# Performance work log

Measured on AMD Instinct MI355X. Metric: run time of the kernel, lower is better.

Reference implementation:

```python
import jax, jax.numpy as jnp
import numpy as np

LN_EPS = 1e-5
N_HEADS = 8

def _layernorm(x, g, b):
    mu = jnp.mean(x, axis=-1, keepdims=True)
    var = jnp.var(x, axis=-1, keepdims=True)
    return (x - mu) * jax.lax.rsqrt(var + LN_EPS) * g + b

def _posenc(seqlen, d_model, dtype):
    den = jnp.exp(-jnp.arange(0, d_model, 2, dtype=dtype) * (np.log(10000.0) / d_model))
    pos = jnp.arange(seqlen, dtype=dtype)[:, None]  # [S,1]
    pe = jnp.zeros((seqlen, d_model), dtype=dtype)
    pe = pe.at[:, 0::2].set(jnp.sin(pos * den))
    pe = pe.at[:, 1::2].set(jnp.cos(pos * den)[:, : d_model // 2])
    return pe  # [S,d]

def setup_inputs() -> dict:
    key = jax.random.key(0)
    ks = jax.random.split(key, 12)
    B, S, V, D, F, L, DL = 64, 256, 16, 512, 2048, 6, 256
    s = 0.05
    return {
        "src_pad": jax.random.normal(ks[0], (B, S, V), jnp.float32),
        "emb_w": jax.random.normal(ks[1], (D, V), jnp.float32) * s,
        "emb_b": jnp.zeros((D,), jnp.float32),
        "qkv_w": jax.random.normal(ks[2], (L, 3 * D, D), jnp.float32) * s,
        "qkv_b": jnp.zeros((L, 3 * D), jnp.float32),
        "out_w": jax.random.normal(ks[3], (L, D, D), jnp.float32) * s,
        "out_b": jnp.zeros((L, D), jnp.float32),
        "ff1_w": jax.random.normal(ks[4], (L, F, D), jnp.float32) * s,
        "ff1_b": jnp.zeros((L, F), jnp.float32),
        "ff2_w": jax.random.normal(ks[5], (L, D, F), jnp.float32) * s,
        "ff2_b": jnp.zeros((L, D), jnp.float32),
        "ln1_g": jnp.ones((L, D), jnp.float32),
        "ln1_b": jnp.zeros((L, D), jnp.float32),
        "ln2_g": jnp.ones((L, D), jnp.float32),
        "ln2_b": jnp.zeros((L, D), jnp.float32),
        "lat_w": jax.random.normal(ks[6], (DL, S * D), jnp.float32) * 0.005,
        "lat_b": jnp.zeros((DL,), jnp.float32),
        "head_w": jax.random.normal(ks[7], (1, DL), jnp.float32) * s,
        "head_b": jnp.zeros((1,), jnp.float32),
    }

def reference(src_pad, emb_w, emb_b, qkv_w, qkv_b, out_w, out_b,
              ff1_w, ff1_b, ff2_w, ff2_b, ln1_g, ln1_b, ln2_g, ln2_b,
              lat_w, lat_b, head_w, head_b):
    B, S, V = src_pad.shape
    D = emb_w.shape[0]
    L = qkv_w.shape[0]
    H = N_HEADS
    dh = D // H
    # batched replacement of the per-token Python-loop embedding
    x = jnp.einsum('bsv,dv->bsd', src_pad, emb_w) + emb_b
    x = x + _posenc(S, D, x.dtype)  # dropout is identity at eval
    scale = 1.0 / np.sqrt(dh)
    for l in range(L):  # post-norm PyTorch TransformerEncoderLayer, relu FFN
        qkv = jnp.einsum('bsd,ed->bse', x, qkv_w[l]) + qkv_b[l]  # [B,S,3D]
        q, k, v = jnp.split(qkv, 3, axis=-1)
        q = q.reshape(B, S, H, dh).transpose(0, 2, 1, 3)
        k = k.reshape(B, S, H, dh).transpose(0, 2, 1, 3)
        v = v.reshape(B, S, H, dh).transpose(0, 2, 1, 3)
        attn = jax.nn.softmax(jnp.einsum('bhqd,bhkd->bhqk', q, k) * scale, axis=-1)
        o = jnp.einsum('bhqk,bhkd->bhqd', attn, v).transpose(0, 2, 1, 3).reshape(B, S, D)
        o = jnp.einsum('bsd,ed->bse', o, out_w[l]) + out_b[l]
        x = _layernorm(x + o, ln1_g[l], ln1_b[l])
        h = jax.nn.relu(jnp.einsum('bsd,fd->bsf', x, ff1_w[l]) + ff1_b[l])
        h = jnp.einsum('bsf,df->bsd', h, ff2_w[l]) + ff2_b[l]
        x = _layernorm(x + h, ln2_g[l], ln2_b[l])
    mem = x.reshape(B, S * D) @ lat_w.T + lat_b  # [B, d_latent]
    pred = jax.nn.sigmoid(mem @ head_w.T + head_b)  # [B,1]
    return pred
```

## Files before the change

kernel.cpp:

```cpp
#include <hip/hip_runtime.h>
#include <hip/hip_bf16.h>
#include <cstdint>

#define DEV static __device__ __forceinline__

typedef __attribute__((ext_vector_type(8))) short bf16x8;
typedef __attribute__((ext_vector_type(4))) float f32x4;

DEV unsigned short f2bf(float f) {
  union { float f; unsigned u; } c; c.f = f;
  unsigned u = c.u;
  return (unsigned short)((u + 0x7fffu + ((u >> 16) & 1u)) >> 16);
}
DEV float bf2f(unsigned short h) {
  union { unsigned u; float f; } c; c.u = ((unsigned)h) << 16; return c.f;
}
DEV float bflo(unsigned u) { union { unsigned u; float f; } c; c.u = u << 16; return c.f; }
DEV float bfhi(unsigned u) { union { unsigned u; float f; } c; c.u = u & 0xffff0000u; return c.f; }
DEV unsigned pack_bf16(float a, float b) {
  union { float f; unsigned u; } ca, cb; ca.f = a; cb.f = b;
  return __builtin_amdgcn_perm(cb.u + 0x8000u, ca.u + 0x8000u, 0x07060302u);
}

#define ASYNC_COPY16(gsrc, ldst)                                                      \
  __builtin_amdgcn_global_load_lds(                                                   \
      (const __attribute__((address_space(1))) void*)(unsigned long long)(gsrc),      \
      (__attribute__((address_space(3))) void*)(unsigned int)(unsigned long long)(ldst), \
      16, 0, 0)

__global__ void cvt4_kernel(const float* __restrict__ s, unsigned short* __restrict__ d) {
  size_t i = ((size_t)blockIdx.x * 256 + threadIdx.x) * 4;
  float4 v = *(const float4*)(s + i);
  d[i + 0] = f2bf(v.x);
  d[i + 1] = f2bf(v.y);
  d[i + 2] = f2bf(v.z);
  d[i + 3] = f2bf(v.w);
}

__global__ void embed_kernel(const float* __restrict__ src,
                             const float* __restrict__ emb_w,
                             const float* __restrict__ emb_b,
                             unsigned short* __restrict__ xb) {
  const int bs = blockIdx.x;
  const int d = threadIdx.x;
  const int s = bs & 255;
  __shared__ float sv[16];
  if (d < 16) sv[d] = src[(size_t)bs * 16 + d];
  __syncthreads();
  const float* wr = emb_w + (size_t)d * 16;
  float acc = emb_b[d];
#pragma unroll
  for (int v = 0; v < 16; v++) acc += sv[v] * wr[v];
  const float den = __expf(-(float)(d & ~1) * (9.2103403719761836f / 512.f));
  const float arg = (float)s * den;
  acc += (d & 1) ? __cosf(arg) : __sinf(arg);
  xb[(size_t)bs * 512 + d] = f2bf(acc);
}

template <int BM, int RELU, int OUT_BF16, int ADD_RES>
__global__ __launch_bounds__(512, 2) void gemm_pipe(
    const unsigned short* __restrict__ A,
    const unsigned short* __restrict__ B,
    const float* __restrict__ bias,
    const unsigned short* __restrict__ res,
    float* __restrict__ Cf,
    unsigned short* __restrict__ Cb,
    int M, int N, int K) {
  constexpr int BN = 256;
  constexpr int MT = BM / 32;
  constexpr int NT = 4;
  constexpr int NLA = BM / 64;
  constexpr int NL = NLA + BN / 64;
  constexpr int BUFE = (BM + BN) * 64;
  __shared__ unsigned short lds[3 * BUFE];

  const int tid = threadIdx.x;
  const int lane = tid & 63;
  const int w = tid >> 6;
  const int wmi = w >> 2;
  const int wni = w & 3;
  const int r16 = lane & 15;
  const int quad = lane >> 4;
  const int rsw = r16 & 7;
  const int m0 = blockIdx.x * BM;
  const int n0 = blockIdx.y * BN;

  const int srow = tid >> 3;
  const int scol = ((tid & 7) ^ (srow & 7)) * 8;
  const unsigned short* gA = A + (size_t)(m0 + srow) * K + scol;
  const unsigned short* gB = B + (size_t)(n0 + srow) * K + scol;

#define STG(i, bufi, kc)                                                        \
  do {                                                                          \
    if ((i) < NLA)                                                              \
      ASYNC_COPY16(gA + (size_t)((i) * 64) * K + (kc),                          \
                   lds + (bufi) * BUFE + ((i) * 64 + w * 8) * 64);              \
    else                                                                        \
      ASYNC_COPY16(gB + (size_t)(((i) - NLA) * 64) * K + (kc),                  \
                   lds + (bufi) * BUFE + (BM + ((i) - NLA) * 64 + w * 8) * 64); \
  } while (0)

  f32x4 acc[MT][NT] = {};

  const int NK = K >> 6;
#pragma unroll
  for (int i = 0; i < NL; ++i) STG(i, 0, 0);
#pragma unroll
  for (int i = 0; i < NL; ++i) STG(i, 1, 64);

  for (int kt = 0; kt < NK; ++kt) {
    const int buf = kt % 3;
    if (kt + 1 < NK)
      asm volatile("s_waitcnt vmcnt(%0)" ::"i"(NL) : "memory");
    else
      asm volatile("s_waitcnt vmcnt(0)" ::: "memory");
    __builtin_amdgcn_s_barrier();
    if (kt + 2 < NK) {
      const int sb = (kt + 2) % 3;
      const int kc = (kt + 2) << 6;
#pragma unroll
      for (int i = 0; i < NL; ++i) STG(i, sb, kc);
    }
    const unsigned short* As = lds + buf * BUFE;
    const unsigned short* Bs = As + BM * 64;
#pragma unroll
    for (int kh = 0; kh < 2; ++kh) {
      const int ko = ((kh * 4 + quad) ^ rsw) * 8;
      bf16x8 aR[MT], bR[NT];
#pragma unroll
      for (int m = 0; m < MT; ++m)
        aR[m] = *(const bf16x8*)(As + (wmi * 64 + m * 16 + r16) * 64 + ko);
#pragma unroll
      for (int j = 0; j < NT; ++j)
        bR[j] = *(const bf16x8*)(Bs + (wni * 64 + j * 16 + r16) * 64 + ko);
      __builtin_amdgcn_s_setprio(1);
#pragma unroll
      for (int m = 0; m < MT; ++m)
#pragma unroll
        for (int j = 0; j < NT; ++j)
          acc[m][j] = __builtin_amdgcn_mfma_f32_16x16x32_bf16(
              bR[j], aR[m], acc[m][j], 0, 0, 0);
      __builtin_amdgcn_s_setprio(0);
    }
    asm volatile("s_waitcnt lgkmcnt(0)" ::: "memory");
  }
#undef STG

  const int mb = m0 + wmi * 64 + r16;
  const int nb = n0 + wni * 64 + quad * 4;
#pragma unroll
  for (int j = 0; j < NT; ++j) {
    const int n = nb + j * 16;
    const float4 bv = *(const float4*)(bias + n);
#pragma unroll
    for (int i = 0; i < MT; ++i) {
      const size_t off = (size_t)(mb + i * 16) * N + n;
      float4 v;
      v.x = acc[i][j][0] + bv.x;
      v.y = acc[i][j][1] + bv.y;
      v.z = acc[i][j][2] + bv.z;
      v.w = acc[i][j][3] + bv.w;
      if (ADD_RES) {
        const uint2 ru = *(const uint2*)(res + off);
        v.x += bflo(ru.x); v.y += bfhi(ru.x);
        v.z += bflo(ru.y); v.w += bfhi(ru.y);
      }
      if (RELU) {
        v.x = fmaxf(v.x, 0.f); v.y = fmaxf(v.y, 0.f);
        v.z = fmaxf(v.z, 0.f); v.w = fmaxf(v.w, 0.f);
      }
      if (OUT_BF16) {
        uint2 u;
        u.x = pack_bf16(v.x, v.y);
        u.y = pack_bf16(v.z, v.w);
        *(uint2*)(Cb + off) = u;
      } else {
        *(float4*)(Cf + off) = v;
      }
    }
  }
}

__global__ __launch_bounds__(256, 2) void attn_fused(
    const unsigned short* __restrict__ qkv,
    unsigned short* __restrict__ O) {
  __shared__ unsigned short Vt[64 * 264];
  __shared__ unsigned short Pl[32 * 264];
  __shared__ float redM[4][32];
  __shared__ float redS[4][32];
  const int tid = threadIdx.x;
  const int lane = tid & 63;
  const int w = tid >> 6;
  const int r16 = lane & 15;
  const int quad = lane >> 4;
  const int h = blockIdx.x & 7;
  const int b = blockIdx.x >> 3;

  {
    const int kp = w * 32 + (lane & 31);
    const int dhalf = lane >> 5;
    const unsigned short* vbase =
        qkv + (size_t)(b * 256 + 2 * kp) * 1536 + 1024 + h * 64;
    unsigned* dst = (unsigned*)Vt;
#pragma unroll
    for (int t = 0; t < 4; t++) {
      const int dc = dhalf + 2 * t;
      const uint4 a = *(const uint4*)(vbase + dc * 8);
      const uint4 bb = *(const uint4*)(vbase + 1536 + dc * 8);
      const unsigned* ap = (const unsigned*)&a;
      const unsigned* bp = (const unsigned*)&bb;
#pragma unroll
      for (int i = 0; i < 4; i++) {
        const unsigned lo = ap[i], hi = bp[i];
        dst[(dc * 8 + 2 * i) * 132 + kp] = (lo & 0xffffu) | (hi << 16);
        dst[(dc * 8 + 2 * i + 1) * 132 + kp] = (lo >> 16) | (hi & 0xffff0000u);
      }
    }
  }
  __syncthreads();

  const unsigned short* krow =
      qkv + (size_t)(b * 256 + r16) * 1536 + 512 + h * 64 + quad * 8;
  const unsigned short* qrow =
      qkv + (size_t)(b * 256 + r16) * 1536 + h * 64 + quad * 8;

  for (int qt = 0; qt < 8; qt++) {
    const int q0 = qt * 32;
    f32x4 acc[4][2] = {};
    bf16x8 bQ0[2], bQ1[2];
#pragma unroll
    for (int nt = 0; nt < 2; nt++) {
      const unsigned short* qp = qrow + (size_t)(q0 + nt * 16) * 1536;
      bQ0[nt] = *(const bf16x8*)(qp);
      bQ1[nt] = *(const bf16x8*)(qp + 32);
    }
#pragma unroll
    for (int mt = 0; mt < 4; mt++) {
      const unsigned short* kp = krow + (size_t)(w * 64 + mt * 16) * 1536;
      const bf16x8 aK0 = *(const bf16x8*)(kp);
      const bf16x8 aK1 = *(const bf16x8*)(kp + 32);
#pragma unroll
      for (int nt = 0; nt < 2; nt++) {
        acc[mt][nt] = __builtin_amdgcn_mfma_f32_16x16x32_bf16(aK0, bQ0[nt], acc[mt][nt], 0, 0, 0);
        acc[mt][nt] = __builtin_amdgcn_mfma_f32_16x16x32_bf16(aK1, bQ1[nt], acc[mt][nt], 0, 0, 0);
      }
    }
#pragma unroll
    for (int nt = 0; nt < 2; nt++) {
      float m = acc[0][nt][0];
#pragma unroll
      for (int mt = 0; mt < 4; mt++)
#pragma unroll
        for (int r = 0; r < 4; r++) m = fmaxf(m, acc[mt][nt][r]);
      m = fmaxf(m, __shfl_xor(m, 16));
      m = fmaxf(m, __shfl_xor(m, 32));
      if (quad == 0) redM[w][nt * 16 + r16] = m;
    }
    __syncthreads();
    float mg[2], sw[2];
#pragma unroll
    for (int nt = 0; nt < 2; nt++) {
      const int q = nt * 16 + r16;
      mg[nt] = fmaxf(fmaxf(redM[0][q], redM[1][q]), fmaxf(redM[2][q], redM[3][q]));
      sw[nt] = 0.f;
    }
#pragma unroll
    for (int mt = 0; mt < 4; mt++)
#pragma unroll
      for (int nt = 0; nt < 2; nt++)
#pragma unroll
        for (int r = 0; r < 4; r++) {
          acc[mt][nt][r] = __expf((acc[mt][nt][r] - mg[nt]) * 0.125f);
          sw[nt] += acc[mt][nt][r];
        }
#pragma unroll
    for (int nt = 0; nt < 2; nt++) {
      sw[nt] += __shfl_xor(sw[nt], 16);
      sw[nt] += __shfl_xor(sw[nt], 32);
      if (quad == 0) redS[w][nt * 16 + r16] = sw[nt];
    }
    __syncthreads();
    float inv[2];
#pragma unroll
    for (int nt = 0; nt < 2; nt++) {
      const int q = nt * 16 + r16;
      inv[nt] = 1.f / (redS[0][q] + redS[1][q] + redS[2][q] + redS[3][q]);
    }
#pragma unroll
    for (int nt = 0; nt < 2; nt++) {
      unsigned short* prow = Pl + (nt * 16 + r16) * 264 + w * 64 + quad * 4;
#pragma unroll
      for (int mt = 0; mt < 4; mt++) {
        uint2 u;
        u.x = pack_bf16(acc[mt][nt][0] * inv[nt], acc[mt][nt][1] * inv[nt]);
        u.y = pack_bf16(acc[mt][nt][2] * inv[nt], acc[mt][nt][3] * inv[nt]);
        *(uint2*)(prow + mt * 16) = u;
      }
    }
    __syncthreads();
    f32x4 o[2] = {};
#pragma unroll
    for (int s = 0; s < 8; s++) {
      const bf16x8 aV = *(const bf16x8*)(Vt + (w * 16 + r16) * 264 + s * 32 + quad * 8);
#pragma unroll
      for (int nt = 0; nt < 2; nt++) {
        const bf16x8 bP = *(const bf16x8*)(Pl + (nt * 16 + r16) * 264 + s * 32 + quad * 8);
        o[nt] = __builtin_amdgcn_mfma_f32_16x16x32_bf16(aV, bP, o[nt], 0, 0, 0);
      }
    }
#pragma unroll
    for (int nt = 0; nt < 2; nt++) {
      uint2 u;
      u.x = pack_bf16(o[nt][0], o[nt][1]);
      u.y = pack_bf16(o[nt][2], o[nt][3]);
      *(uint2*)(O + (size_t)(b * 256 + q0 + nt * 16 + r16) * 512 + h * 64 +
                w * 16 + quad * 4) = u;
    }
  }
}

__global__ __launch_bounds__(256) void ln_kernel(
    const float* __restrict__ z, const float* __restrict__ g,
    const float* __restrict__ bb, unsigned short* __restrict__ xb) {
  const int row = blockIdx.x;
  const int tid = threadIdx.x;
  const size_t base = (size_t)row * 512;
  float v0 = z[base + tid];
  float v1 = z[base + tid + 256];
  float s = v0 + v1, ss = v0 * v0 + v1 * v1;
#pragma unroll
  for (int off = 32; off > 0; off >>= 1) {
    s += __shfl_xor(s, off);
    ss += __shfl_xor(ss, off);
  }
  __shared__ float red[8];
  const int w = tid >> 6, lane = tid & 63;
  if (lane == 0) { red[w * 2] = s; red[w * 2 + 1] = ss; }
  __syncthreads();
  s = red[0] + red[2] + red[4] + red[6];
  ss = red[1] + red[3] + red[5] + red[7];
  const float mu = s * (1.f / 512.f);
  const float var = ss * (1.f / 512.f) - mu * mu;
  const float rs = rsqrtf(var + 1e-5f);
  const float o0 = (v0 - mu) * rs * g[tid] + bb[tid];
  const float o1 = (v1 - mu) * rs * g[tid + 256] + bb[tid + 256];
  xb[base + tid] = f2bf(o0);
  xb[base + tid + 256] = f2bf(o1);
}

__global__ void zero_kernel(float* __restrict__ p) {
  p[blockIdx.x * 256 + threadIdx.x] = 0.f;
}

__global__ __launch_bounds__(256) void latent_gemm(
    const unsigned short* __restrict__ xb, const float* __restrict__ W,
    float* __restrict__ mem) {
  const int tid = threadIdx.x;
  const int lane = tid & 63;
  const int w = tid >> 6;
  const int r16 = lane & 15;
  const int quad = lane >> 4;
  const int n0 = blockIdx.x * 64 + w * 16;
  const int kc0 = blockIdx.y * 1024;

  const float* wrow = W + (size_t)(n0 + r16) * 131072 + kc0 + quad * 8;
  const unsigned short* xrow = xb + (size_t)r16 * 131072 + kc0 + quad * 8;

  f32x4 c[4] = {};
  for (int k = 0; k < 1024; k += 32) {
    const float4 wa = *(const float4*)(wrow + k);
    const float4 wb = *(const float4*)(wrow + k + 4);
    union { unsigned u[4]; bf16x8 v; } cw;
    cw.u[0] = pack_bf16(wa.x, wa.y);
    cw.u[1] = pack_bf16(wa.z, wa.w);
    cw.u[2] = pack_bf16(wb.x, wb.y);
    cw.u[3] = pack_bf16(wb.z, wb.w);
#pragma unroll
    for (int i = 0; i < 4; i++) {
      const bf16x8 aX = *(const bf16x8*)(xrow + (size_t)i * 2097152 + k);
      c[i] = __builtin_amdgcn_mfma_f32_16x16x32_bf16(aX, cw.v, c[i], 0, 0, 0);
    }
  }
#pragma unroll
  for (int i = 0; i < 4; i++)
#pragma unroll
    for (int r = 0; r < 4; r++)
      atomicAdd(&mem[(size_t)(i * 16 + quad * 4 + r) * 256 + n0 + r16], c[i][r]);
}

__global__ __launch_bounds__(256) void head_kernel(
    const float* __restrict__ mem, const float* __restrict__ lat_b,
    const float* __restrict__ head_w, const float* __restrict__ head_b,
    float* __restrict__ out) {
  const int b = blockIdx.x;
  const int tid = threadIdx.x;
  float v = (mem[(size_t)b * 256 + tid] + lat_b[tid]) * head_w[tid];
#pragma unroll
  for (int off = 32; off > 0; off >>= 1) v += __shfl_xor(v, off);
  __shared__ float red[4];
  const int w = tid >> 6, lane = tid & 63;
  if (lane == 0) red[w] = v;
  __syncthreads();
  if (tid == 0) {
    const float z = red[0] + red[1] + red[2] + red[3] + head_b[0];
    out[b] = 1.f / (1.f + __expf(-z));
  }
}

extern "C" void kernel_launch(void* const* d_in, const int* in_sizes, int n_in,
                              void* d_out, int out_size, void* d_ws, size_t ws_size,
                              hipStream_t stream) {
  (void)in_sizes; (void)n_in; (void)out_size; (void)ws_size;
  const float* src_pad = (const float*)d_in[0];
  const float* emb_w = (const float*)d_in[1];
  const float* emb_b = (const float*)d_in[2];
  const float* qkv_w = (const float*)d_in[3];
  const float* qkv_b = (const float*)d_in[4];
  const float* out_w = (const float*)d_in[5];
  const float* out_b = (const float*)d_in[6];
  const float* ff1_w = (const float*)d_in[7];
  const float* ff1_b = (const float*)d_in[8];
  const float* ff2_w = (const float*)d_in[9];
  const float* ff2_b = (const float*)d_in[10];
  const float* ln1_g = (const float*)d_in[11];
  const float* ln1_b = (const float*)d_in[12];
  const float* ln2_g = (const float*)d_in[13];
  const float* ln2_b = (const float*)d_in[14];
  const float* lat_w = (const float*)d_in[15];
  const float* lat_b = (const float*)d_in[16];
  const float* head_w = (const float*)d_in[17];
  const float* head_b = (const float*)d_in[18];
  float* out = (float*)d_out;

  char* p = (char*)d_ws;
  unsigned short* xb = (unsigned short*)p; p += (size_t)16384 * 512 * 2;
  unsigned short* qkv = (unsigned short*)p;
  float* y = (float*)qkv;
  p += (size_t)16384 * 1536 * 2;
  unsigned short* attno = (unsigned short*)p; p += (size_t)16384 * 512 * 2;
  unsigned short* h = (unsigned short*)p;     p += (size_t)16384 * 2048 * 2;
  unsigned short* wq = (unsigned short*)p;    p += (size_t)4718592 * 2;
  unsigned short* wo = (unsigned short*)p;    p += (size_t)1572864 * 2;
  unsigned short* wf1 = (unsigned short*)p;   p += (size_t)6291456 * 2;
  unsigned short* wf2 = (unsigned short*)p;   p += (size_t)6291456 * 2;
  float* mem = (float*)p;           p += (size_t)16384 * 4;

  cvt4_kernel<<<4608, 256, 0, stream>>>(qkv_w, wq);
  cvt4_kernel<<<1536, 256, 0, stream>>>(out_w, wo);
  cvt4_kernel<<<6144, 256, 0, stream>>>(ff1_w, wf1);
  cvt4_kernel<<<6144, 256, 0, stream>>>(ff2_w, wf2);

  embed_kernel<<<16384, 512, 0, stream>>>(src_pad, emb_w, emb_b, xb);

  for (int l = 0; l < 6; l++) {
    gemm_pipe<128, 0, 1, 0><<<dim3(128, 6), 512, 0, stream>>>(
        xb, wq + (size_t)l * 786432, qkv_b + (size_t)l * 1536, nullptr,
        nullptr, qkv, 16384, 1536, 512);
    attn_fused<<<512, 256, 0, stream>>>(qkv, attno);
    gemm_pipe<128, 0, 0, 1><<<dim3(128, 2), 512, 0, stream>>>(
        attno, wo + (size_t)l * 262144, out_b + (size_t)l * 512, xb,
        y, nullptr, 16384, 512, 512);
    ln_kernel<<<16384, 256, 0, stream>>>(y, ln1_g + (size_t)l * 512,
                                         ln1_b + (size_t)l * 512, xb);
    gemm_pipe<128, 1, 1, 0><<<dim3(128, 8), 512, 0, stream>>>(
        xb, wf1 + (size_t)l * 1048576, ff1_b + (size_t)l * 2048, nullptr,
        nullptr, h, 16384, 2048, 512);
    gemm_pipe<128, 0, 0, 1><<<dim3(128, 2), 512, 0, stream>>>(
        h, wf2 + (size_t)l * 1048576, ff2_b + (size_t)l * 512, xb,
        y, nullptr, 16384, 512, 2048);
    ln_kernel<<<16384, 256, 0, stream>>>(y, ln2_g + (size_t)l * 512,
                                         ln2_b + (size_t)l * 512, xb);
  }

  zero_kernel<<<64, 256, 0, stream>>>(mem);
  latent_gemm<<<dim3(4, 128), 256, 0, stream>>>(xb, lat_w, mem);
  head_kernel<<<64, 256, 0, stream>>>(mem, lat_b, head_w, head_b, out);
}
```

Before: 1.584 ms.

## Fuse residual add and LayerNorm into out-proj and FF2 GEMM epilogues

Adds a gemm_ln kernel where each block computes a full 512-wide output row tile, so bias, residual add and LayerNorm statistics are reduced in the epilogue and bf16 results are written back directly. This removes the fp32 intermediate buffer and the separate LayerNorm kernels, saving memory traffic and launches. The four weight-conversion launches are also merged into one. The new kernel uses a large LDS footprint with only double buffering and a smaller M tile, which may reduce latency hiding.

```diff
diff --git a/kernel.cpp b/kernel.cpp
--- a/kernel.cpp
+++ b/kernel.cpp
@@ -28,8 +28,17 @@
       (__attribute__((address_space(3))) void*)(unsigned int)(unsigned long long)(ldst), \
       16, 0, 0)
 
-__global__ void cvt4_kernel(const float* __restrict__ s, unsigned short* __restrict__ d) {
-  size_t i = ((size_t)blockIdx.x * 256 + threadIdx.x) * 4;
+__global__ void cvt_all_kernel(const float* __restrict__ s0, unsigned short* __restrict__ d0,
+                               const float* __restrict__ s1, unsigned short* __restrict__ d1,
+                               const float* __restrict__ s2, unsigned short* __restrict__ d2,
+                               const float* __restrict__ s3, unsigned short* __restrict__ d3) {
+  const int blk = blockIdx.x;
+  const float* s; unsigned short* d; int base;
+  if (blk < 4608)       { s = s0; d = d0; base = blk; }
+  else if (blk < 6144)  { s = s1; d = d1; base = blk - 4608; }
+  else if (blk < 12288) { s = s2; d = d2; base = blk - 6144; }
+  else                  { s = s3; d = d3; base = blk - 12288; }
+  size_t i = ((size_t)base * 256 + threadIdx.x) * 4;
   float4 v = *(const float4*)(s + i);
   d[i + 0] = f2bf(v.x);
   d[i + 1] = f2bf(v.y);
@@ -57,13 +66,11 @@
   xb[(size_t)bs * 512 + d] = f2bf(acc);
 }
 
-template <int BM, int RELU, int OUT_BF16, int ADD_RES>
+template <int BM, int RELU>
 __global__ __launch_bounds__(512, 2) void gemm_pipe(
     const unsigned short* __restrict__ A,
     const unsigned short* __restrict__ B,
     const float* __restrict__ bias,
-    const unsigned short* __restrict__ res,
-    float* __restrict__ Cf,
     unsigned short* __restrict__ Cb,
     int M, int N, int K) {
   constexpr int BN = 256;
@@ -160,23 +167,168 @@
       v.y = acc[i][j][1] + bv.y;
       v.z = acc[i][j][2] + bv.z;
       v.w = acc[i][j][3] + bv.w;
-      if (ADD_RES) {
-        const uint2 ru = *(const uint2*)(res + off);
-        v.x += bflo(ru.x); v.y += bfhi(ru.x);
-        v.z += bflo(ru.y); v.w += bfhi(ru.y);
-      }
       if (RELU) {
         v.x = fmaxf(v.x, 0.f); v.y = fmaxf(v.y, 0.f);
         v.z = fmaxf(v.z, 0.f); v.w = fmaxf(v.w, 0.f);
       }
-      if (OUT_BF16) {
-        uint2 u;
-        u.x = pack_bf16(v.x, v.y);
-        u.y = pack_bf16(v.z, v.w);
-        *(uint2*)(Cb + off) = u;
-      } else {
-        *(float4*)(Cf + off) = v;
+      uint2 u;
+      u.x = pack_bf16(v.x, v.y);
+      u.y = pack_bf16(v.z, v.w);
+      *(uint2*)(Cb + off) = u;
+    }
+  }
+}
+
+__global__ __launch_bounds__(512, 2) void gemm_ln(
+    const unsigned short* __restrict__ A,
+    const unsigned short* __restrict__ B,
+    const float* __restrict__ bias,
+    const float* __restrict__ g,
+    const float* __restrict__ beta,
+    unsigned short* __restrict__ xb,
+    int K) {
+  constexpr int BM = 64;
+  constexpr int MT = 4;
+  constexpr int NT = 4;
+  constexpr int NL = 1 + 8;
+  constexpr int BUFE = (BM + 512) * 64;
+  __shared__ unsigned short lds[2 * BUFE];
+
+  const int tid = threadIdx.x;
+  const int lane = tid & 63;
+  const int w = tid >> 6;
+  const int r16 = lane & 15;
+  const int quad = lane >> 4;
+  const int rsw = r16 & 7;
+  const int m0 = blockIdx.x * BM;
+
+  const int srow = tid >> 3;
+  const int scol = ((tid & 7) ^ (srow & 7)) * 8;
+  const unsigned short* gA = A + (size_t)(m0 + srow) * K + scol;
+  const unsigned short* gB = B + (size_t)srow * K + scol;
+
+#define STG2(i, bufi, kc)                                                       \
+  do {                                                                          \
+    if ((i) == 0)                                                               \
+      ASYNC_COPY16(gA + (size_t)(kc), lds + (bufi) * BUFE + (w * 8) * 64);      \
+    else                                                                        \
+      ASYNC_COPY16(gB + (size_t)(((i) - 1) * 64) * K + (kc),                    \
+                   lds + (bufi) * BUFE + (BM + ((i) - 1) * 64 + w * 8) * 64);   \
+  } while (0)
+
+  f32x4 acc[MT][NT] = {};
+
+  const int NK = K >> 6;
+#pragma unroll
+  for (int i = 0; i < NL; ++i) STG2(i, 0, 0);
+
+  for (int kt = 0; kt < NK; ++kt) {
+    const int buf = kt & 1;
+    if (kt + 1 < NK) {
+      const int kc = (kt + 1) << 6;
+#pragma unroll
+      for (int i = 0; i < NL; ++i) STG2(i, buf ^ 1, kc);
+      asm volatile("s_waitcnt vmcnt(%0)" ::"i"(NL) : "memory");
+    } else {
+      asm volatile("s_waitcnt vmcnt(0)" ::: "memory");
+    }
+    __builtin_amdgcn_s_barrier();
+    const unsigned short* As = lds + buf * BUFE;
+    const unsigned short* Bs = As + BM * 64;
+#pragma unroll
+    for (int kh = 0; kh < 2; ++kh) {
+      const int ko = ((kh * 4 + quad) ^ rsw) * 8;
+      bf16x8 aR[MT], bR[NT];
+#pragma unroll
+      for (int m = 0; m < MT; ++m)
+        aR[m] = *(const bf16x8*)(As + (m * 16 + r16) * 64 + ko);
+#pragma unroll
+      for (int j = 0; j < NT; ++j)
+        bR[j] = *(const bf16x8*)(Bs + (w * 64 + j * 16 + r16) * 64 + ko);
+      __builtin_amdgcn_s_setprio(1);
+#pragma unroll
+      for (int m = 0; m < MT; ++m)
+#pragma unroll
+        for (int j = 0; j < NT; ++j)
+          acc[m][j] = __builtin_amdgcn_mfma_f32_16x16x32_bf16(
+              bR[j], aR[m], acc[m][j], 0, 0, 0);
+      __builtin_amdgcn_s_setprio(0);
+    }
+    asm volatile("s_waitcnt lgkmcnt(0)" ::: "memory");
+    __builtin_amdgcn_s_barrier();
+  }
+#undef STG2
+
+  const int nb = w * 64 + quad * 4;
+  float psum[MT] = {}, psq[MT] = {};
+#pragma unroll
+  for (int j = 0; j < NT; ++j) {
+    const int n = nb + j * 16;
+    const float4 bv = *(const float4*)(bias + n);
+#pragma unroll
+    for (int i = 0; i < MT; ++i) {
+      const size_t off = (size_t)(m0 + i * 16 + r16) * 512 + n;
+      const uint2 ru = *(const uint2*)(xb + off);
+      f32x4 v;
+      v[0] = acc[i][j][0] + bv.x + bflo(ru.x);
+      v[1] = acc[i][j][1] + bv.y + bfhi(ru.x);
+      v[2] = acc[i][j][2] + bv.z + bflo(ru.y);
+      v[3] = acc[i][j][3] + bv.w + bfhi(ru.y);
+      acc[i][j] = v;
+#pragma unroll
+      for (int r = 0; r < 4; ++r) {
+        psum[i] += v[r];
+        psq[i] += v[r] * v[r];
       }
+    }
+  }
+#pragma unroll
+  for (int i = 0; i < MT; ++i) {
+    psum[i] += __shfl_xor(psum[i], 16);
+    psum[i] += __shfl_xor(psum[i], 32);
+    psq[i] += __shfl_xor(psq[i], 16);
+    psq[i] += __shfl_xor(psq[i], 32);
+  }
+  float* redS = (float*)lds;
+  float* redQ = redS + 512;
+  if (quad == 0) {
+#pragma unroll
+    for (int i = 0; i < MT; ++i) {
+      redS[w * 64 + i * 16 + r16] = psum[i];
+      redQ[w * 64 + i * 16 + r16] = psq[i];
+    }
+  }
+  __syncthreads();
+  float mu[MT], rs[MT];
+#pragma unroll
+  for (int i = 0; i < MT; ++i) {
+    const int row = i * 16 + r16;
+    float s = 0.f, q = 0.f;
+#pragma unroll
+    for (int ww = 0; ww < 8; ++ww) {
+      s += redS[ww * 64 + row];
+      q += redQ[ww * 64 + row];
+    }
+    mu[i] = s * (1.f / 512.f);
+    rs[i] = rsqrtf(q * (1.f / 512.f) - mu[i] * mu[i] + 1e-5f);
+  }
+#pragma unroll
+  for (int j = 0; j < NT; ++j) {
+    const int n = nb + j * 16;
+    const float4 gv = *(const float4*)(g + n);
+    const float4 be = *(const float4*)(beta + n);
+#pragma unroll
+    for (int i = 0; i < MT; ++i) {
+      const size_t off = (size_t)(m0 + i * 16 + r16) * 512 + n;
+      const f32x4 v = acc[i][j];
+      float o0 = (v[0] - mu[i]) * rs[i] * gv.x + be.x;
+      float o1 = (v[1] - mu[i]) * rs[i] * gv.y + be.y;
+      float o2 = (v[2] - mu[i]) * rs[i] * gv.z + be.z;
+      float o3 = (v[3] - mu[i]) * rs[i] * gv.w + be.w;
+      uint2 u;
+      u.x = pack_bf16(o0, o1);
+      u.y = pack_bf16(o2, o3);
+      *(uint2*)(xb + off) = u;
     }
   }
 }
@@ -317,35 +469,6 @@
                 w * 16 + quad * 4) = u;
     }
   }
-}
-
-__global__ __launch_bounds__(256) void ln_kernel(
-    const float* __restrict__ z, const float* __restrict__ g,
-    const float* __restrict__ bb, unsigned short* __restrict__ xb) {
-  const int row = blockIdx.x;
-  const int tid = threadIdx.x;
-  const size_t base = (size_t)row * 512;
-  float v0 = z[base + tid];
-  float v1 = z[base + tid + 256];
-  float s = v0 + v1, ss = v0 * v0 + v1 * v1;
-#pragma unroll
-  for (int off = 32; off > 0; off >>= 1) {
-    s += __shfl_xor(s, off);
-    ss += __shfl_xor(ss, off);
-  }
-  __shared__ float red[8];
-  const int w = tid >> 6, lane = tid & 63;
-  if (lane == 0) { red[w * 2] = s; red[w * 2 + 1] = ss; }
-  __syncthreads();
-  s = red[0] + red[2] + red[4] + red[6];
-  ss = red[1] + red[3] + red[5] + red[7];
-  const float mu = s * (1.f / 512.f);
-  const float var = ss * (1.f / 512.f) - mu * mu;
-  const float rs = rsqrtf(var + 1e-5f);
-  const float o0 = (v0 - mu) * rs * g[tid] + bb[tid];
-  const float o1 = (v1 - mu) * rs * g[tid + 256] + bb[tid + 256];
-  xb[base + tid] = f2bf(o0);
-  xb[base + tid + 256] = f2bf(o1);
 }
 
 __global__ void zero_kernel(float* __restrict__ p) {
@@ -434,9 +557,7 @@
 
   char* p = (char*)d_ws;
   unsigned short* xb = (unsigned short*)p; p += (size_t)16384 * 512 * 2;
-  unsigned short* qkv = (unsigned short*)p;
-  float* y = (float*)qkv;
-  p += (size_t)16384 * 1536 * 2;
+  unsigned short* qkv = (unsigned short*)p; p += (size_t)16384 * 1536 * 2;
   unsigned short* attno = (unsigned short*)p; p += (size_t)16384 * 512 * 2;
   unsigned short* h = (unsigned short*)p;     p += (size_t)16384 * 2048 * 2;
   unsigned short* wq = (unsigned short*)p;    p += (size_t)4718592 * 2;
@@ -445,31 +566,25 @@
   unsigned short* wf2 = (unsigned short*)p;   p += (size_t)6291456 * 2;
   float* mem = (float*)p;           p += (size_t)16384 * 4;
 
-  cvt4_kernel<<<4608, 256, 0, stream>>>(qkv_w, wq);
-  cvt4_kernel<<<1536, 256, 0, stream>>>(out_w, wo);
-  cvt4_kernel<<<6144, 256, 0, stream>>>(ff1_w, wf1);
-  cvt4_kernel<<<6144, 256, 0, stream>>>(ff2_w, wf2);
+  cvt_all_kernel<<<18432, 256, 0, stream>>>(qkv_w, wq, out_w, wo, ff1_w, wf1,
+                                            ff2_w, wf2);
 
   embed_kernel<<<16384, 512, 0, stream>>>(src_pad, emb_w, emb_b, xb);
 
   for (int l = 0; l < 6; l++) {
-    gemm_pipe<128, 0, 1, 0><<<dim3(128, 6), 512, 0, stream>>>(
-        xb, wq + (size_t)l * 786432, qkv_b + (size_t)l * 1536, nullptr,
-        nullptr, qkv, 16384, 1536, 512);
+    gemm_pipe<128, 0><<<dim3(128, 6), 512, 0, stream>>>(
+        xb, wq + (size_t)l * 786432, qkv_b + (size_t)l * 1536, qkv,
+        16384, 1536, 512);
     attn_fused<<<512, 256, 0, stream>>>(qkv, attno);
-    gemm_pipe<128, 0, 0, 1><<<dim3(128, 2), 512, 0, stream>>>(
-        attno, wo + (size_t)l * 262144, out_b + (size_t)l * 512, xb,
-        y, nullptr, 16384, 512, 512);
-    ln_kernel<<<16384, 256, 0, stream>>>(y, ln1_g + (size_t)l * 512,
-                                         ln1_b + (size_t)l * 512, xb);
-    gemm_pipe<128, 1, 1, 0><<<dim3(128, 8), 512, 0, stream>>>(
-        xb, wf1 + (size_t)l * 1048576, ff1_b + (size_t)l * 2048, nullptr,
-        nullptr, h, 16384, 2048, 512);
-    gemm_pipe<128, 0, 0, 1><<<dim3(128, 2), 512, 0, stream>>>(
-        h, wf2 + (size_t)l * 1048576, ff2_b + (size_t)l * 512, xb,
-        y, nullptr, 16384, 512, 2048);
-    ln_kernel<<<16384, 256, 0, stream>>>(y, ln2_g + (size_t)l * 512,
-                                         ln2_b + (size_t)l * 512, xb);
+    gemm_ln<<<256, 512, 0, stream>>>(
+        attno, wo + (size_t)l * 262144, out_b + (size_t)l * 512,
+        ln1_g + (size_t)l * 512, ln1_b + (size_t)l * 512, xb, 512);
+    gemm_pipe<128, 1><<<dim3(128, 8), 512, 0, stream>>>(
+        xb, wf1 + (size_t)l * 1048576, ff1_b + (size_t)l * 2048, h,
+        16384, 2048, 512);
+    gemm_ln<<<256, 512, 0, stream>>>(
+        h, wf2 + (size_t)l * 1048576, ff2_b + (size_t)l * 512,
+        ln2_g + (size_t)l * 512, ln2_b + (size_t)l * 512, xb, 2048);
   }
 
   zero_kernel<<<64, 256, 0, stream>>>(mem);
```

Result: faster. 1.534 ms (-3.2%).
